# Performance work log

Measured on AMD Instinct MI355X. Metric: run time of the kernel, lower is better.

The kernel has to match this reference:

```python
import jax, jax.numpy as jnp
import numpy as np

B, N, C_IN, C_OUT, K = 2, 8192, 128, 128, 21  # K = num_neighbors + 1 (self)
EPS = 1e-5

def knn_idx(xyz, k):
    # xyz: [B,N,3] -> idx [B,N,k] of k nearest neighbors (self included)
    d2 = jnp.sum(xyz * xyz, axis=-1)  # [B,N]
    dist = d2[:, :, None] + d2[:, None, :] - 2.0 * jnp.einsum('bnd,bmd->bnm', xyz, xyz)
    _, idx = jax.lax.top_k(-dist, k)
    return idx

def group_points(pts, idx):
    # pts [B,N,D], idx [B,N,K] -> [B,N,K,D]
    return jax.vmap(lambda p, i: p[i])(pts, idx)

def group_feats(f, idx):
    # f [B,C,N], idx [B,N,K] -> [B,C,N,K]
    return jax.vmap(lambda ff, i: ff[:, i])(f, idx)

def conv_bn_relu(x, W, g, b, m, v):
    # 1x1 conv (bias=False) + BatchNorm (inference stats) + ReLU
    y = jnp.einsum('oc,bcnk->bonk', W, x)
    inv = g / jnp.sqrt(v + EPS)
    return jax.nn.relu(y * inv[None, :, None, None] + (b - m * inv)[None, :, None, None])

def setup_inputs():
    key = jax.random.key(0)
    ks = jax.random.split(key, 12)
    return {
        'xyz': jax.random.normal(ks[0], (B, N, 3), jnp.float32),
        'f': jax.random.normal(ks[1], (B, C_IN, N), jnp.float32),
        'W_geo': jax.random.normal(ks[2], (C_OUT, 6), jnp.float32) * 0.1,
        'g_geo': jax.random.uniform(ks[3], (C_OUT,), jnp.float32, 0.5, 1.5),
        'b_geo': jax.random.normal(ks[4], (C_OUT,), jnp.float32) * 0.1,
        'm_geo': jax.random.normal(ks[5], (C_OUT,), jnp.float32) * 0.1,
        'v_geo': jax.random.uniform(ks[6], (C_OUT,), jnp.float32, 0.5, 1.5),
        'W_feat': jax.random.normal(ks[7], (C_OUT, 2 * C_IN), jnp.float32) * 0.05,
        'g_feat': jax.random.uniform(ks[8], (C_OUT,), jnp.float32, 0.5, 1.5),
        'b_feat': jax.random.normal(ks[9], (C_OUT,), jnp.float32) * 0.1,
        'm_feat': jax.random.normal(ks[10], (C_OUT,), jnp.float32) * 0.1,
        'v_feat': jax.random.uniform(ks[11], (C_OUT,), jnp.float32, 0.5, 1.5),
    }

def reference(xyz, f, W_geo, g_geo, b_geo, m_geo, v_geo, W_feat, g_feat, b_feat, m_feat, v_feat):
    idx = knn_idx(xyz, K)                                   # [B,N,K]
    grouped_xyz = group_points(xyz, idx)                    # [B,N,K,3]
    xyz_diff = jnp.transpose(grouped_xyz - xyz[:, :, None, :], (0, 3, 1, 2))  # [B,3,N,K]
    center = jnp.broadcast_to(jnp.transpose(xyz, (0, 2, 1))[:, :, :, None], (B, 3, N, K))
    G_geo = jnp.concatenate([center, xyz_diff], axis=1)     # [B,6,N,K]
    grouped_f = group_feats(f, idx)                         # [B,C,N,K]
    center_f = jnp.broadcast_to(f[:, :, :, None], (B, C_IN, N, K))
    G_feat = jnp.concatenate([center_f, grouped_f - center_f], axis=1)  # [B,2C,N,K]
    G_geo = conv_bn_relu(G_geo, W_geo, g_geo, b_geo, m_geo, v_geo)      # [B,C_OUT,N,K]
    G_feat = conv_bn_relu(G_feat, W_feat, g_feat, b_feat, m_feat, v_feat)
    feature = jnp.concatenate([G_geo, G_feat], axis=1)      # [B,2*C_OUT,N,K]
    return jnp.max(feature, axis=-1)                        # [B,2*C_OUT,N]
```

## Files before the change

### kernel.cpp

```cpp
#include <hip/hip_runtime.h>

typedef unsigned int u32;
typedef unsigned long long u64;
typedef unsigned short u16;

#define DEV __device__ __forceinline__

DEV u16 f2bf(float x) {
  u32 u = __float_as_uint(x);
  u32 r = u + 0x7fffu + ((u >> 16) & 1u);
  return (u16)(r >> 16);
}
DEV float bflo(u32 d) { return __uint_as_float(d << 16); }
DEV float bfhi(u32 d) { return __uint_as_float(d & 0xffff0000u); }
DEV u64 sortable64(double f) {
  long long b = __double_as_longlong(f);
  return (u64)b ^ (u64)((b >> 63) | (long long)0x8000000000000000ll);
}
DEV double ddist(double qx, double qy, double qz, double qd2,
                 float mxf, float myf, float mzf) {
  double cx = (double)mxf, cy = (double)myf, cz = (double)mzf;
  double cd2 = cx * cx + cy * cy + cz * cz;
  double dot = cx * qx + cy * qy + cz * qz;
  return (qd2 + cd2) - 2.0 * dot;
}

#define NB 2
#define NN 8192
#define NC 128
#define KK 21
#define MARGIN 1e-3f
#define CT 2048

__global__ __launch_bounds__(256) void k_prep(
    const float* __restrict__ Wf, const float* __restrict__ gf, const float* __restrict__ bf_,
    const float* __restrict__ mf, const float* __restrict__ vf,
    const float* __restrict__ Wg, const float* __restrict__ gg, const float* __restrict__ bg,
    const float* __restrict__ mg, const float* __restrict__ vg,
    u16* __restrict__ Wt, float* __restrict__ beta_f,
    float* __restrict__ Wgu, float* __restrict__ Wgv, float* __restrict__ beta_g) {
  int g = blockIdx.x * 256 + threadIdx.x;
  int c = g >> 8, o = g & 255;
  float val;
  if (o < 128) {
    float inv = gf[o] / sqrtf(vf[o] + 1e-5f);
    val = inv * (Wf[o * 256 + c] - Wf[o * 256 + c + 128]);
  } else {
    int o2 = o - 128;
    float inv = gf[o2] / sqrtf(vf[o2] + 1e-5f);
    val = inv * Wf[o2 * 256 + c + 128];
  }
  Wt[c * 256 + o] = f2bf(val);
  if (g < 128) {
    float inv = gf[g] / sqrtf(vf[g] + 1e-5f);
    beta_f[g] = bf_[g] - mf[g] * inv;
  } else if (g < 256) {
    int oo = g - 128;
    float invg = gg[oo] / sqrtf(vg[oo] + 1e-5f);
#pragma unroll
    for (int d = 0; d < 3; ++d) {
      Wgu[oo * 3 + d] = invg * (Wg[oo * 6 + d] - Wg[oo * 6 + 3 + d]);
      Wgv[oo * 3 + d] = invg * Wg[oo * 6 + 3 + d];
    }
    beta_g[oo] = bg[oo] - mg[oo] * invg;
  }
}

__global__ __launch_bounds__(256) void k_geo(
    const float* __restrict__ xyz, const float* __restrict__ Wgu, const float* __restrict__ Wgv,
    const float* __restrict__ beta_g, u32* __restrict__ ucat, u32* __restrict__ vcat) {
  int g = blockIdx.x * 256 + threadIdx.x;
  int p = g >> 6, oc = g & 63;
  const float* xp = xyz + p * 3;
  float X = xp[0], Y = xp[1], Z = xp[2];
  u32 du = 0, dv = 0;
#pragma unroll
  for (int h = 0; h < 2; ++h) {
    int o = oc * 2 + h;
    float ug = X * Wgu[o * 3] + Y * Wgu[o * 3 + 1] + Z * Wgu[o * 3 + 2] + beta_g[o];
    float vv = X * Wgv[o * 3] + Y * Wgv[o * 3 + 1] + Z * Wgv[o * 3 + 2];
    du |= (u32)f2bf(ug) << (16 * h);
    dv |= (u32)f2bf(vv) << (16 * h);
  }
  ucat[p * 128 + oc] = du;
  vcat[p * 128 + oc] = dv;
}

__global__ __launch_bounds__(256) void k_feat(
    const float* __restrict__ f, const u32* __restrict__ Wt32, const float* __restrict__ beta_f,
    u32* __restrict__ ucat, u32* __restrict__ vcat) {
  __shared__ u32 sW[128 * 128];
  __shared__ float sF[128][68];

  const int t = threadIdx.x;
  const int b = blockIdx.x >> 7;
  const int n0 = (blockIdx.x & 127) << 6;
  const int boff = b * (NC * NN);

#pragma unroll
  for (int k = 0; k < 64; ++k) sW[t + (k << 8)] = Wt32[t + (k << 8)];
#pragma unroll
  for (int k = 0; k < 32; ++k) {
    int i = t + (k << 8);
    int c = i >> 6, col = i & 63;
    sF[c][col] = f[boff + c * NN + n0 + col];
  }
  __syncthreads();

  const int w = t >> 6, lane = t & 63;
  const int og = lane >> 3, pg = lane & 7;
  const int o0 = w * 64 + og * 8;
  const int p0 = pg * 8;

  float acc[8][8];
#pragma unroll
  for (int a = 0; a < 8; ++a)
#pragma unroll
    for (int p = 0; p < 8; ++p) acc[a][p] = 0.0f;

  for (int c = 0; c < 128; ++c) {
    float4 fa = *(const float4*)&sF[c][p0];
    float4 fb = *(const float4*)&sF[c][p0 + 4];
    uint4 wr = *(const uint4*)&sW[c * 128 + (o0 >> 1)];
    float wv[8] = {bflo(wr.x), bfhi(wr.x), bflo(wr.y), bfhi(wr.y),
                   bflo(wr.z), bfhi(wr.z), bflo(wr.w), bfhi(wr.w)};
    float fv[8] = {fa.x, fa.y, fa.z, fa.w, fb.x, fb.y, fb.z, fb.w};
#pragma unroll
    for (int a = 0; a < 8; ++a)
#pragma unroll
      for (int p = 0; p < 8; ++p) acc[a][p] = __builtin_fmaf(wv[a], fv[p], acc[a][p]);
  }

  const int ochan = o0 & 127;
  const bool is_u = (o0 < 128);
  float bet[8];
#pragma unroll
  for (int a = 0; a < 8; ++a) bet[a] = is_u ? beta_f[ochan + a] : 0.0f;
  u32* dstbase = is_u ? ucat : vcat;
#pragma unroll
  for (int p = 0; p < 8; ++p) {
    int pt = (b << 13) + n0 + p0 + p;
    u32 d0 = (u32)f2bf(acc[0][p] + bet[0]) | ((u32)f2bf(acc[1][p] + bet[1]) << 16);
    u32 d1 = (u32)f2bf(acc[2][p] + bet[2]) | ((u32)f2bf(acc[3][p] + bet[3]) << 16);
    u32 d2 = (u32)f2bf(acc[4][p] + bet[4]) | ((u32)f2bf(acc[5][p] + bet[5]) << 16);
    u32 d3 = (u32)f2bf(acc[6][p] + bet[6]) | ((u32)f2bf(acc[7][p] + bet[7]) << 16);
    *(uint4*)&dstbase[pt * 128 + 64 + (ochan >> 1)] = make_uint4(d0, d1, d2, d3);
  }
}

__global__ __launch_bounds__(256, 4) void k_knn(const float* __restrict__ xyz,
                                                int* __restrict__ knn) {
  __shared__ float4 sc[CT];
  __shared__ u16 ssurv[16][128];
  __shared__ u32 scnt[16];

  const int t = threadIdx.x;
  const int blk = blockIdx.x;
  const int b = blk >> 9;
  const int n0 = (blk & 511) << 4;
  const float* X = xyz + b * (NN * 3);

  if (t < 16) scnt[t] = 0u;

  const int w = t >> 6, lane = t & 63;

  float mx[4], my[4], mz[4];
#pragma unroll
  for (int i = 0; i < 4; ++i) {
    int q = n0 + (w << 2) + i;
    mx[i] = -2.0f * X[q * 3];
    my[i] = -2.0f * X[q * 3 + 1];
    mz[i] = -2.0f * X[q * 3 + 2];
  }

  float mn[4];
#pragma unroll
  for (int i = 0; i < 4; ++i) mn[i] = __builtin_inff();

  for (int ct = 0; ct < NN / CT; ++ct) {
    __syncthreads();
    const float* Xt = X + ct * (CT * 3);
#pragma unroll
    for (int k = 0; k < 8; ++k) {
      int c = (k << 8) + t;
      float x = Xt[c * 3], y = Xt[c * 3 + 1], z = Xt[c * 3 + 2];
      float d2 = __builtin_fmaf(x, x, __builtin_fmaf(y, y, z * z));
      sc[c] = make_float4(x, y, z, d2);
    }
    __syncthreads();
#pragma unroll 4
    for (int cc = 0; cc < CT; cc += 64) {
      float4 C = sc[cc + lane];
#pragma unroll
      for (int i = 0; i < 4; ++i) {
        float s = __builtin_fmaf(C.x, mx[i],
                  __builtin_fmaf(C.y, my[i],
                  __builtin_fmaf(C.z, mz[i], C.w)));
        mn[i] = fminf(mn[i], s);
      }
    }
  }

  float thr[4];
#pragma unroll
  for (int i = 0; i < 4; ++i) {
    float v = mn[i];
#pragma unroll
    for (int k = 2; k <= 64; k <<= 1) {
#pragma unroll
      for (int j = k >> 1; j > 0; j >>= 1) {
        float p = __shfl_xor(v, j);
        bool takeMin = (((lane & k) == 0) == ((lane & j) == 0));
        v = takeMin ? fminf(v, p) : fmaxf(v, p);
      }
    }
    thr[i] = __shfl(v, 20) + MARGIN;
  }

  for (int ct = 0; ct < NN / CT; ++ct) {
    __syncthreads();
    const float* Xt = X + ct * (CT * 3);
#pragma unroll
    for (int k = 0; k < 8; ++k) {
      int c = (k << 8) + t;
      float x = Xt[c * 3], y = Xt[c * 3 + 1], z = Xt[c * 3 + 2];
      float d2 = __builtin_fmaf(x, x, __builtin_fmaf(y, y, z * z));
      sc[c] = make_float4(x, y, z, d2);
    }
    __syncthreads();
    int mbase = ct * CT + lane;
#pragma unroll 4
    for (int cc = 0; cc < CT; cc += 64) {
      float4 C = sc[cc + lane];
#pragma unroll
      for (int i = 0; i < 4; ++i) {
        float s = __builtin_fmaf(C.x, mx[i],
                  __builtin_fmaf(C.y, my[i],
                  __builtin_fmaf(C.z, mz[i], C.w)));
        if (s <= thr[i]) {
          int qq = (w << 2) + i;
          u32 slot = atomicAdd(&scnt[qq], 1u);
          if (slot < 128u) ssurv[qq][slot] = (u16)(mbase + cc);
        }
      }
    }
  }
  __syncthreads();

#pragma unroll 1
  for (int i = 0; i < 4; ++i) {
    const int qq = (w << 2) + i;
    const int q = n0 + qq;
    double Qx = (double)X[q * 3], Qy = (double)X[q * 3 + 1], Qz = (double)X[q * 3 + 2];
    double Qd2 = Qx * Qx + Qy * Qy + Qz * Qz;
    u32 cnt = scnt[qq];
    int* outp = knn + ((b << 13) + q) * KK;

    bool v0 = ((u32)lane < cnt);
    u32 m0 = v0 ? (u32)ssurv[qq][lane] : 0u;
    double s0 = ddist(Qx, Qy, Qz, Qd2, X[m0 * 3], X[m0 * 3 + 1], X[m0 * 3 + 2]);
    u64 k0 = v0 ? ((sortable64(s0) & 0xFFFFFFFFFFFFE000ull) | (u64)m0) : ~0ull;

    if (cnt <= 64u) {
      u64 v = k0;
#pragma unroll
      for (int k = 2; k <= 64; k <<= 1) {
#pragma unroll
        for (int j = k >> 1; j > 0; j >>= 1) {
          u64 p = __shfl_xor(v, j);
          bool takeMin = (((lane & k) == 0) == ((lane & j) == 0));
          bool pl = p < v;
          u64 mnv = pl ? p : v;
          u64 mxv = pl ? v : p;
          v = takeMin ? mnv : mxv;
        }
      }
      if (lane < KK) outp[lane] = (int)(v & 8191ull);
    } else {
      bool v1 = ((u32)(lane + 64) < cnt);
      u32 m1 = v1 ? (u32)ssurv[qq][lane + 64] : 0u;
      double s1 = ddist(Qx, Qy, Qz, Qd2, X[m1 * 3], X[m1 * 3 + 1], X[m1 * 3 + 2]);
      u64 k1 = v1 ? ((sortable64(s1) & 0xFFFFFFFFFFFFE000ull) | (u64)m1) : ~0ull;
      u32 selm = 0;
      for (int r = 0; r < KK; ++r) {
        u64 mk = (k0 < k1) ? k0 : k1;
#pragma unroll
        for (int j = 32; j > 0; j >>= 1) {
          u64 p = __shfl_xor(mk, j);
          if (p < mk) mk = p;
        }
        if (k0 == mk) k0 = ~0ull;
        else if (k1 == mk) k1 = ~0ull;
        if (lane == r) selm = (u32)(mk & 8191ull);
      }
      if (lane < KK) outp[lane] = (int)selm;
    }
  }
}

__global__ __launch_bounds__(256) void k_gather(
    const u32* __restrict__ ucat, const u32* __restrict__ vcat,
    const int* __restrict__ knn, float* __restrict__ out) {
  __shared__ float tr[64 * 258];

  const int t = threadIdx.x;
  const int b = blockIdx.x >> 7;
  const int n0 = (blockIdx.x & 127) << 6;
  const int w = t >> 6, lane = t & 63;
  const int which = w >> 1;
  const int lo = ((w & 1) << 6) | lane;

  for (int step = 0; step < 32; ++step) {
    int qq = step * 2 + which;
    int q = n0 + qq;
    const int* ip = knn + ((b << 13) + q) * KK;
    float a0 = -__builtin_inff(), a1 = -__builtin_inff();
#pragma unroll
    for (int k = 0; k < KK; ++k) {
      int p = ip[k];
      u32 d = vcat[(((b << 13) + p) << 7) + lo];
      a0 = fmaxf(a0, bflo(d));
      a1 = fmaxf(a1, bfhi(d));
    }
    u32 u = ucat[(((b << 13) + q) << 7) + lo];
    float r0 = fmaxf(bflo(u) + a0, 0.0f);
    float r1 = fmaxf(bfhi(u) + a1, 0.0f);
    *(float2*)&tr[qq * 258 + 2 * lo] = make_float2(r0, r1);
  }
  __syncthreads();

  float* ob = out + b * (256 * NN);
  for (int i = 0; i < 64; ++i) {
    int o = (w << 6) + i;
    ob[o * NN + n0 + lane] = tr[lane * 258 + o];
  }
}

extern "C" void kernel_launch(void* const* d_in, const int* in_sizes, int n_in,
                              void* d_out, int out_size, void* d_ws, size_t ws_size,
                              hipStream_t stream) {
  const float* xyz = (const float*)d_in[0];
  const float* f   = (const float*)d_in[1];
  const float* Wg  = (const float*)d_in[2];
  const float* gg  = (const float*)d_in[3];
  const float* bg  = (const float*)d_in[4];
  const float* mg  = (const float*)d_in[5];
  const float* vg  = (const float*)d_in[6];
  const float* Wf  = (const float*)d_in[7];
  const float* gf  = (const float*)d_in[8];
  const float* bf_ = (const float*)d_in[9];
  const float* mf  = (const float*)d_in[10];
  const float* vf  = (const float*)d_in[11];

  char* ws = (char*)d_ws;
  u16*   Wt     = (u16*)ws;
  float* beta_f = (float*)(ws + 65536);
  float* Wgu    = (float*)(ws + 66048);
  float* Wgv    = (float*)(ws + 67584);
  float* beta_g = (float*)(ws + 69120);
  u32*   ucat   = (u32*)(ws + 69632);
  u32*   vcat   = (u32*)(ws + 69632 + 8388608);
  int*   knn    = (int*)(ws + 69632 + 2 * 8388608);
  float* out    = (float*)d_out;

  if (ws_size < (size_t)(69632 + 2 * 8388608 + 16384 * KK * 4)) return;

  k_prep<<<dim3(128), dim3(256), 0, stream>>>(Wf, gf, bf_, mf, vf, Wg, gg, bg, mg, vg,
                                              Wt, beta_f, Wgu, Wgv, beta_g);
  k_geo<<<dim3(4096), dim3(256), 0, stream>>>(xyz, Wgu, Wgv, beta_g, ucat, vcat);
  k_feat<<<dim3(256), dim3(256), 0, stream>>>(f, (const u32*)Wt, beta_f, ucat, vcat);
  k_knn<<<dim3(1024), dim3(256), 0, stream>>>(xyz, knn);
  k_gather<<<dim3(256), dim3(256), 0, stream>>>(ucat, vcat, knn, out);
}
```

Before: 194.2 us.

## Compute kNN distance filtering with bf16 split-precision MFMA instead of scalar FMA

Adds a packing kernel that splits each point's coordinates and squared norm into hi/lo bf16 parts. The kNN kernel then computes the candidate distance matrix for 32 queries per block with 32x32x16 bf16 MFMA instructions, replacing per-lane scalar FMAs over LDS-staged tiles. It uses that matrix both for the 21st-smallest threshold pass and for the survivor-collection pass. Because the split bf16 distances are approximate, the margin is widened and the survivor buffer grows to 256, with a new 4-key selection path. Exact ranking is still done in double precision. The risk is more survivors and atomics per query, and possible misses if the approximation error exceeds the margin.

After: 205.5 us. 1.06x slower.

```diff
diff --git a/kernel.cpp b/kernel.cpp
--- a/kernel.cpp
+++ b/kernel.cpp
@@ -5,12 +5,16 @@
 typedef unsigned short u16;
 
 #define DEV __device__ __forceinline__
+
+typedef __attribute__((ext_vector_type(8))) short bf16x8;
+typedef __attribute__((ext_vector_type(16))) float f32x16;
 
 DEV u16 f2bf(float x) {
   u32 u = __float_as_uint(x);
   u32 r = u + 0x7fffu + ((u >> 16) & 1u);
   return (u16)(r >> 16);
 }
+DEV float bf2f(u16 h) { return __uint_as_float((u32)h << 16); }
 DEV float bflo(u32 d) { return __uint_as_float(d << 16); }
 DEV float bfhi(u32 d) { return __uint_as_float(d & 0xffff0000u); }
 DEV u64 sortable64(double f) {
@@ -29,8 +33,8 @@
 #define NN 8192
 #define NC 128
 #define KK 21
-#define MARGIN 1e-3f
-#define CT 2048
+#define MARGIN 0.012f
+#define BF16_ONE ((u16)0x3F80)
 
 __global__ __launch_bounds__(256) void k_prep(
     const float* __restrict__ Wf, const float* __restrict__ gf, const float* __restrict__ bf_,
@@ -148,63 +152,104 @@
   }
 }
 
-__global__ __launch_bounds__(256, 4) void k_knn(const float* __restrict__ xyz,
+__global__ __launch_bounds__(256) void k_pack(const float* __restrict__ xyz,
+                                              u16* __restrict__ pack) {
+  int p = blockIdx.x * 256 + threadIdx.x;
+  const float* xp = xyz + p * 3;
+  float x = xp[0], y = xp[1], z = xp[2];
+  u16 hx = f2bf(x), hy = f2bf(y), hz = f2bf(z);
+  u16 lx = f2bf(x - bf2f(hx)), ly = f2bf(y - bf2f(hy)), lz = f2bf(z - bf2f(hz));
+  float cd2 = __builtin_fmaf(x, x, __builtin_fmaf(y, y, z * z));
+  u16 dh = f2bf(cd2), dl = f2bf(cd2 - bf2f(dh));
+
+  int g = p >> 5, n = p & 31;
+  u32* h0 = (u32*)(pack + (size_t)g * 512 + n * 8);
+  u32* h1 = (u32*)(pack + (size_t)g * 512 + 256 + n * 8);
+  h0[0] = (u32)hx | ((u32)hy << 16);
+  h0[1] = (u32)hz | ((u32)hx << 16);
+  h0[2] = (u32)hy | ((u32)hz << 16);
+  h0[3] = (u32)lx | ((u32)ly << 16);
+  h1[0] = (u32)lz | ((u32)dh << 16);
+  h1[1] = (u32)dl | ((u32)lx << 16);
+  h1[2] = (u32)ly | ((u32)lz << 16);
+  h1[3] = 0u;
+}
+
+DEV u64 surv_key(const u16* __restrict__ srow, u32 cnt, int pos,
+                 const float* __restrict__ X,
+                 double Qx, double Qy, double Qz, double Qd2) {
+  bool vv = (u32)pos < cnt;
+  u32 m = vv ? (u32)srow[pos] : 0u;
+  double ss = ddist(Qx, Qy, Qz, Qd2, X[m * 3], X[m * 3 + 1], X[m * 3 + 2]);
+  return vv ? ((sortable64(ss) & 0xFFFFFFFFFFFFE000ull) | (u64)m) : ~0ull;
+}
+
+__global__ __launch_bounds__(256, 2) void k_knn(const float* __restrict__ xyz,
+                                                const u16* __restrict__ pack,
                                                 int* __restrict__ knn) {
-  __shared__ float4 sc[CT];
-  __shared__ u16 ssurv[16][128];
-  __shared__ u32 scnt[16];
-
-  const int t = threadIdx.x;
+  __shared__ float smin[32][128];
+  __shared__ u16 ssurv[32][256];
+  __shared__ float sthr[32];
+  __shared__ u32 scnt[32];
+
+  const int t = threadIdx.x, w = t >> 6, lane = t & 63;
   const int blk = blockIdx.x;
-  const int b = blk >> 9;
-  const int n0 = (blk & 511) << 4;
+  const int b = blk >> 8;
+  const int n0 = (blk & 255) << 5;
   const float* X = xyz + b * (NN * 3);
-
-  if (t < 16) scnt[t] = 0u;
-
-  const int w = t >> 6, lane = t & 63;
-
-  float mx[4], my[4], mz[4];
-#pragma unroll
-  for (int i = 0; i < 4; ++i) {
-    int q = n0 + (w << 2) + i;
-    mx[i] = -2.0f * X[q * 3];
-    my[i] = -2.0f * X[q * 3 + 1];
-    mz[i] = -2.0f * X[q * 3 + 2];
-  }
-
-  float mn[4];
-#pragma unroll
-  for (int i = 0; i < 4; ++i) mn[i] = __builtin_inff();
-
-  for (int ct = 0; ct < NN / CT; ++ct) {
-    __syncthreads();
-    const float* Xt = X + ct * (CT * 3);
-#pragma unroll
-    for (int k = 0; k < 8; ++k) {
-      int c = (k << 8) + t;
-      float x = Xt[c * 3], y = Xt[c * 3 + 1], z = Xt[c * 3 + 2];
-      float d2 = __builtin_fmaf(x, x, __builtin_fmaf(y, y, z * z));
-      sc[c] = make_float4(x, y, z, d2);
-    }
-    __syncthreads();
-#pragma unroll 4
-    for (int cc = 0; cc < CT; cc += 64) {
-      float4 C = sc[cc + lane];
-#pragma unroll
-      for (int i = 0; i < 4; ++i) {
-        float s = __builtin_fmaf(C.x, mx[i],
-                  __builtin_fmaf(C.y, my[i],
-                  __builtin_fmaf(C.z, mz[i], C.w)));
-        mn[i] = fminf(mn[i], s);
-      }
-    }
-  }
-
-  float thr[4];
-#pragma unroll
-  for (int i = 0; i < 4; ++i) {
-    float v = mn[i];
+  const u16* PB = pack + (size_t)b * NN * 16;
+
+  if (t < 32) scnt[t] = 0u;
+
+  const int mq = lane & 31, h = lane >> 5;
+  union { u16 u[8]; bf16x8 v; } afr;
+  {
+    int q = n0 + mq;
+    float qx = -2.0f * X[q * 3], qy = -2.0f * X[q * 3 + 1], qz = -2.0f * X[q * 3 + 2];
+    u16 hx = f2bf(qx), hy = f2bf(qy), hz = f2bf(qz);
+    u16 lx = f2bf(qx - bf2f(hx)), ly = f2bf(qy - bf2f(hy)), lz = f2bf(qz - bf2f(hz));
+    if (h == 0) {
+      afr.u[0] = hx; afr.u[1] = hy; afr.u[2] = hz; afr.u[3] = lx;
+      afr.u[4] = ly; afr.u[5] = lz; afr.u[6] = hx; afr.u[7] = hy;
+    } else {
+      afr.u[0] = hz; afr.u[1] = BF16_ONE; afr.u[2] = BF16_ONE; afr.u[3] = lx;
+      afr.u[4] = ly; afr.u[5] = lz; afr.u[6] = 0; afr.u[7] = 0;
+    }
+  }
+
+  f32x16 zacc = {0.f, 0.f, 0.f, 0.f, 0.f, 0.f, 0.f, 0.f,
+                 0.f, 0.f, 0.f, 0.f, 0.f, 0.f, 0.f, 0.f};
+
+  float mn[16];
+#pragma unroll
+  for (int r = 0; r < 16; ++r) mn[r] = __builtin_inff();
+
+  for (int i0 = 0; i0 < 64; i0 += 8) {
+    uint4 braw[8];
+#pragma unroll
+    for (int j = 0; j < 8; ++j) {
+      int tile = w + 4 * (i0 + j);
+      braw[j] = *(const uint4*)(PB + (size_t)tile * 512 + lane * 8);
+    }
+#pragma unroll
+    for (int j = 0; j < 8; ++j) {
+      union { uint4 r; bf16x8 v; } bf; bf.r = braw[j];
+      f32x16 d = __builtin_amdgcn_mfma_f32_32x32x16_bf16(afr.v, bf.v, zacc, 0, 0, 0);
+#pragma unroll
+      for (int r = 0; r < 16; ++r) mn[r] = fminf(mn[r], d[r]);
+    }
+  }
+
+#pragma unroll
+  for (int r = 0; r < 16; ++r) {
+    int row = (r & 3) + 8 * (r >> 2) + 4 * h;
+    smin[row][w * 32 + mq] = mn[r];
+  }
+  __syncthreads();
+
+  for (int i = 0; i < 8; ++i) {
+    int row = w * 8 + i;
+    float v = fminf(smin[row][lane], smin[row][lane + 64]);
 #pragma unroll
     for (int k = 2; k <= 64; k <<= 1) {
 #pragma unroll
@@ -214,33 +259,33 @@
         v = takeMin ? fminf(v, p) : fmaxf(v, p);
       }
     }
-    thr[i] = __shfl(v, 20) + MARGIN;
-  }
-
-  for (int ct = 0; ct < NN / CT; ++ct) {
-    __syncthreads();
-    const float* Xt = X + ct * (CT * 3);
-#pragma unroll
-    for (int k = 0; k < 8; ++k) {
-      int c = (k << 8) + t;
-      float x = Xt[c * 3], y = Xt[c * 3 + 1], z = Xt[c * 3 + 2];
-      float d2 = __builtin_fmaf(x, x, __builtin_fmaf(y, y, z * z));
-      sc[c] = make_float4(x, y, z, d2);
-    }
-    __syncthreads();
-    int mbase = ct * CT + lane;
-#pragma unroll 4
-    for (int cc = 0; cc < CT; cc += 64) {
-      float4 C = sc[cc + lane];
-#pragma unroll
-      for (int i = 0; i < 4; ++i) {
-        float s = __builtin_fmaf(C.x, mx[i],
-                  __builtin_fmaf(C.y, my[i],
-                  __builtin_fmaf(C.z, mz[i], C.w)));
-        if (s <= thr[i]) {
-          int qq = (w << 2) + i;
-          u32 slot = atomicAdd(&scnt[qq], 1u);
-          if (slot < 128u) ssurv[qq][slot] = (u16)(mbase + cc);
+    float t20 = __shfl(v, 20);
+    if (lane == 0) sthr[row] = t20 + MARGIN;
+  }
+  __syncthreads();
+
+  float thr[16];
+#pragma unroll
+  for (int r = 0; r < 16; ++r) thr[r] = sthr[(r & 3) + 8 * (r >> 2) + 4 * h];
+
+  for (int i0 = 0; i0 < 64; i0 += 4) {
+    uint4 braw[4];
+#pragma unroll
+    for (int j = 0; j < 4; ++j) {
+      int tile = w + 4 * (i0 + j);
+      braw[j] = *(const uint4*)(PB + (size_t)tile * 512 + lane * 8);
+    }
+#pragma unroll
+    for (int j = 0; j < 4; ++j) {
+      int tile = w + 4 * (i0 + j);
+      union { uint4 r; bf16x8 v; } bf; bf.r = braw[j];
+      f32x16 d = __builtin_amdgcn_mfma_f32_32x32x16_bf16(afr.v, bf.v, zacc, 0, 0, 0);
+#pragma unroll
+      for (int r = 0; r < 16; ++r) {
+        if (d[r] <= thr[r]) {
+          int row = (r & 3) + 8 * (r >> 2) + 4 * h;
+          u32 slot = atomicAdd(&scnt[row], 1u);
+          if (slot < 256u) ssurv[row][slot] = (u16)(tile * 32 + mq);
         }
       }
     }
@@ -248,18 +293,16 @@
   __syncthreads();
 
 #pragma unroll 1
-  for (int i = 0; i < 4; ++i) {
-    const int qq = (w << 2) + i;
+  for (int i = 0; i < 8; ++i) {
+    const int qq = (w << 3) + i;
     const int q = n0 + qq;
     double Qx = (double)X[q * 3], Qy = (double)X[q * 3 + 1], Qz = (double)X[q * 3 + 2];
     double Qd2 = Qx * Qx + Qy * Qy + Qz * Qz;
-    u32 cnt = scnt[qq];
+    u32 cnt = scnt[qq]; if (cnt > 256u) cnt = 256u;
+    const u16* srow = ssurv[qq];
     int* outp = knn + ((b << 13) + q) * KK;
 
-    bool v0 = ((u32)lane < cnt);
-    u32 m0 = v0 ? (u32)ssurv[qq][lane] : 0u;
-    double s0 = ddist(Qx, Qy, Qz, Qd2, X[m0 * 3], X[m0 * 3 + 1], X[m0 * 3 + 2]);
-    u64 k0 = v0 ? ((sortable64(s0) & 0xFFFFFFFFFFFFE000ull) | (u64)m0) : ~0ull;
+    u64 k0 = surv_key(srow, cnt, lane, X, Qx, Qy, Qz, Qd2);
 
     if (cnt <= 64u) {
       u64 v = k0;
@@ -276,11 +319,8 @@
         }
       }
       if (lane < KK) outp[lane] = (int)(v & 8191ull);
-    } else {
-      bool v1 = ((u32)(lane + 64) < cnt);
-      u32 m1 = v1 ? (u32)ssurv[qq][lane + 64] : 0u;
-      double s1 = ddist(Qx, Qy, Qz, Qd2, X[m1 * 3], X[m1 * 3 + 1], X[m1 * 3 + 2]);
-      u64 k1 = v1 ? ((sortable64(s1) & 0xFFFFFFFFFFFFE000ull) | (u64)m1) : ~0ull;
+    } else if (cnt <= 128u) {
+      u64 k1 = surv_key(srow, cnt, lane + 64, X, Qx, Qy, Qz, Qd2);
       u32 selm = 0;
       for (int r = 0; r < KK; ++r) {
         u64 mk = (k0 < k1) ? k0 : k1;
@@ -291,6 +331,27 @@
         }
         if (k0 == mk) k0 = ~0ull;
         else if (k1 == mk) k1 = ~0ull;
+        if (lane == r) selm = (u32)(mk & 8191ull);
+      }
+      if (lane < KK) outp[lane] = (int)selm;
+    } else {
+      u64 k1 = surv_key(srow, cnt, lane + 64, X, Qx, Qy, Qz, Qd2);
+      u64 k2 = surv_key(srow, cnt, lane + 128, X, Qx, Qy, Qz, Qd2);
+      u64 k3 = surv_key(srow, cnt, lane + 192, X, Qx, Qy, Qz, Qd2);
+      u32 selm = 0;
+      for (int r = 0; r < KK; ++r) {
+        u64 m01 = (k0 < k1) ? k0 : k1;
+        u64 m23 = (k2 < k3) ? k2 : k3;
+        u64 mk = (m01 < m23) ? m01 : m23;
+#pragma unroll
+        for (int j = 32; j > 0; j >>= 1) {
+          u64 p = __shfl_xor(mk, j);
+          if (p < mk) mk = p;
+        }
+        if (k0 == mk) k0 = ~0ull;
+        else if (k1 == mk) k1 = ~0ull;
+        else if (k2 == mk) k2 = ~0ull;
+        else if (k3 == mk) k3 = ~0ull;
         if (lane == r) selm = (u32)(mk & 8191ull);
       }
       if (lane < KK) outp[lane] = (int)selm;
@@ -360,15 +421,17 @@
   float* beta_g = (float*)(ws + 69120);
   u32*   ucat   = (u32*)(ws + 69632);
   u32*   vcat   = (u32*)(ws + 69632 + 8388608);
-  int*   knn    = (int*)(ws + 69632 + 2 * 8388608);
+  int*   knn    = (int*)(ws + 16846848);
+  u16*   pack   = (u16*)(ws + 18223104);
   float* out    = (float*)d_out;
 
-  if (ws_size < (size_t)(69632 + 2 * 8388608 + 16384 * KK * 4)) return;
+  if (ws_size < (size_t)(18223104 + 524288)) return;
 
   k_prep<<<dim3(128), dim3(256), 0, stream>>>(Wf, gf, bf_, mf, vf, Wg, gg, bg, mg, vg,
                                               Wt, beta_f, Wgu, Wgv, beta_g);
   k_geo<<<dim3(4096), dim3(256), 0, stream>>>(xyz, Wgu, Wgv, beta_g, ucat, vcat);
   k_feat<<<dim3(256), dim3(256), 0, stream>>>(f, (const u32*)Wt, beta_f, ucat, vcat);
-  k_knn<<<dim3(1024), dim3(256), 0, stream>>>(xyz, knn);
+  k_pack<<<dim3(64), dim3(256), 0, stream>>>(xyz, pack);
+  k_knn<<<dim3(512), dim3(256), 0, stream>>>(xyz, (const u16*)pack, knn);
   k_gather<<<dim3(256), dim3(256), 0, stream>>>(ucat, vcat, knn, out);
 }
```

## Fuse kNN threshold and survivor passes into single sweep with progressive threshold

Applied to the files above, without the earlier changes.

The kNN kernel previously swept all candidates twice: once to compute a 21st-smallest threshold per query, and again to collect survivors. It now derives an initial threshold from the first 2048-point tile and collects survivors in the same single sweep, tightening the threshold after each later tile. Tile loading also switches to float4-vectorized global reads. Because early thresholds are looser, more candidates survive, so survivor capacity grows to 192 and a three-slot selection path is added. The trade-off is extra atomics and shared-memory traffic, and a risk of overflowing the survivor buffer.

After: 232.1 us. +19.5%, slower.

```diff
diff --git a/kernel.cpp b/kernel.cpp
--- a/kernel.cpp
+++ b/kernel.cpp
@@ -31,6 +31,7 @@
 #define KK 21
 #define MARGIN 1e-3f
 #define CT 2048
+#define SCAP 192
 
 __global__ __launch_bounds__(256) void k_prep(
     const float* __restrict__ Wf, const float* __restrict__ gf, const float* __restrict__ bf_,
@@ -148,10 +149,32 @@
   }
 }
 
+DEV u64 surv_key(const u16* __restrict__ srow, u32 cnt, int pos,
+                 const float* __restrict__ X,
+                 double Qx, double Qy, double Qz, double Qd2) {
+  bool vv = (u32)pos < cnt;
+  u32 m = vv ? (u32)srow[pos] : 0u;
+  double ss = ddist(Qx, Qy, Qz, Qd2, X[m * 3], X[m * 3 + 1], X[m * 3 + 2]);
+  return vv ? ((sortable64(ss) & 0xFFFFFFFFFFFFE000ull) | (u64)m) : ~0ull;
+}
+
+DEV float stat21(float v, int lane) {
+#pragma unroll
+  for (int k = 2; k <= 64; k <<= 1) {
+#pragma unroll
+    for (int j = k >> 1; j > 0; j >>= 1) {
+      float p = __shfl_xor(v, j);
+      bool takeMin = (((lane & k) == 0) == ((lane & j) == 0));
+      v = takeMin ? fminf(v, p) : fmaxf(v, p);
+    }
+  }
+  return __shfl(v, 20);
+}
+
 __global__ __launch_bounds__(256, 4) void k_knn(const float* __restrict__ xyz,
                                                 int* __restrict__ knn) {
   __shared__ float4 sc[CT];
-  __shared__ u16 ssurv[16][128];
+  __shared__ u16 ssurv[16][SCAP];
   __shared__ u32 scnt[16];
 
   const int t = threadIdx.x;
@@ -173,75 +196,102 @@
     mz[i] = -2.0f * X[q * 3 + 2];
   }
 
-  float mn[4];
+  float mn[4], thr[4];
 #pragma unroll
   for (int i = 0; i < 4; ++i) mn[i] = __builtin_inff();
 
-  for (int ct = 0; ct < NN / CT; ++ct) {
+  {
+    const float4* g4 = (const float4*)X;
+#pragma unroll
+    for (int gix = 0; gix < 2; ++gix) {
+      int g = t + (gix << 8);
+      float4 a = g4[g * 3], bb = g4[g * 3 + 1], c = g4[g * 3 + 2];
+      float px[4] = {a.x, a.w, bb.z, c.y};
+      float py[4] = {a.y, bb.x, bb.w, c.z};
+      float pz[4] = {a.z, bb.y, c.x, c.w};
+#pragma unroll
+      for (int j = 0; j < 4; ++j) {
+        float d2 = __builtin_fmaf(px[j], px[j], __builtin_fmaf(py[j], py[j], pz[j] * pz[j]));
+        sc[(g << 2) + j] = make_float4(px[j], py[j], pz[j], d2);
+      }
+    }
+  }
+  __syncthreads();
+
+#pragma unroll 4
+  for (int cc = 0; cc < CT; cc += 64) {
+    float4 C = sc[cc + lane];
+#pragma unroll
+    for (int i = 0; i < 4; ++i) {
+      float s = __builtin_fmaf(C.x, mx[i],
+                __builtin_fmaf(C.y, my[i],
+                __builtin_fmaf(C.z, mz[i], C.w)));
+      mn[i] = fminf(mn[i], s);
+    }
+  }
+#pragma unroll
+  for (int i = 0; i < 4; ++i) thr[i] = stat21(mn[i], lane) + MARGIN;
+
+#pragma unroll 4
+  for (int cc = 0; cc < CT; cc += 64) {
+    float4 C = sc[cc + lane];
+    int mbase = cc + lane;
+#pragma unroll
+    for (int i = 0; i < 4; ++i) {
+      float s = __builtin_fmaf(C.x, mx[i],
+                __builtin_fmaf(C.y, my[i],
+                __builtin_fmaf(C.z, mz[i], C.w)));
+      if (s <= thr[i]) {
+        int qq = (w << 2) + i;
+        u32 slot = atomicAdd(&scnt[qq], 1u);
+        if (slot < (u32)SCAP) ssurv[qq][slot] = (u16)mbase;
+      }
+    }
+  }
+
+  for (int ct = 1; ct < NN / CT; ++ct) {
     __syncthreads();
-    const float* Xt = X + ct * (CT * 3);
-#pragma unroll
-    for (int k = 0; k < 8; ++k) {
-      int c = (k << 8) + t;
-      float x = Xt[c * 3], y = Xt[c * 3 + 1], z = Xt[c * 3 + 2];
-      float d2 = __builtin_fmaf(x, x, __builtin_fmaf(y, y, z * z));
-      sc[c] = make_float4(x, y, z, d2);
+    {
+      const float4* g4 = (const float4*)(X + ct * (CT * 3));
+#pragma unroll
+      for (int gix = 0; gix < 2; ++gix) {
+        int g = t + (gix << 8);
+        float4 a = g4[g * 3], bb = g4[g * 3 + 1], c = g4[g * 3 + 2];
+        float px[4] = {a.x, a.w, bb.z, c.y};
+        float py[4] = {a.y, bb.x, bb.w, c.z};
+        float pz[4] = {a.z, bb.y, c.x, c.w};
+#pragma unroll
+        for (int j = 0; j < 4; ++j) {
+          float d2 = __builtin_fmaf(px[j], px[j], __builtin_fmaf(py[j], py[j], pz[j] * pz[j]));
+          sc[(g << 2) + j] = make_float4(px[j], py[j], pz[j], d2);
+        }
+      }
     }
     __syncthreads();
+
+    int tbase = ct * CT;
 #pragma unroll 4
     for (int cc = 0; cc < CT; cc += 64) {
       float4 C = sc[cc + lane];
+      int mbase = tbase + cc + lane;
 #pragma unroll
       for (int i = 0; i < 4; ++i) {
         float s = __builtin_fmaf(C.x, mx[i],
                   __builtin_fmaf(C.y, my[i],
                   __builtin_fmaf(C.z, mz[i], C.w)));
         mn[i] = fminf(mn[i], s);
-      }
-    }
-  }
-
-  float thr[4];
-#pragma unroll
-  for (int i = 0; i < 4; ++i) {
-    float v = mn[i];
-#pragma unroll
-    for (int k = 2; k <= 64; k <<= 1) {
-#pragma unroll
-      for (int j = k >> 1; j > 0; j >>= 1) {
-        float p = __shfl_xor(v, j);
-        bool takeMin = (((lane & k) == 0) == ((lane & j) == 0));
-        v = takeMin ? fminf(v, p) : fmaxf(v, p);
-      }
-    }
-    thr[i] = __shfl(v, 20) + MARGIN;
-  }
-
-  for (int ct = 0; ct < NN / CT; ++ct) {
-    __syncthreads();
-    const float* Xt = X + ct * (CT * 3);
-#pragma unroll
-    for (int k = 0; k < 8; ++k) {
-      int c = (k << 8) + t;
-      float x = Xt[c * 3], y = Xt[c * 3 + 1], z = Xt[c * 3 + 2];
-      float d2 = __builtin_fmaf(x, x, __builtin_fmaf(y, y, z * z));
-      sc[c] = make_float4(x, y, z, d2);
-    }
-    __syncthreads();
-    int mbase = ct * CT + lane;
-#pragma unroll 4
-    for (int cc = 0; cc < CT; cc += 64) {
-      float4 C = sc[cc + lane];
-#pragma unroll
-      for (int i = 0; i < 4; ++i) {
-        float s = __builtin_fmaf(C.x, mx[i],
-                  __builtin_fmaf(C.y, my[i],
-                  __builtin_fmaf(C.z, mz[i], C.w)));
         if (s <= thr[i]) {
           int qq = (w << 2) + i;
           u32 slot = atomicAdd(&scnt[qq], 1u);
-          if (slot < 128u) ssurv[qq][slot] = (u16)(mbase + cc);
+          if (slot < (u32)SCAP) ssurv[qq][slot] = (u16)mbase;
         }
+      }
+    }
+    if (ct < 3) {
+#pragma unroll
+      for (int i = 0; i < 4; ++i) {
+        float nt = stat21(mn[i], lane) + MARGIN;
+        thr[i] = fminf(thr[i], nt);
       }
     }
   }
@@ -253,13 +303,11 @@
     const int q = n0 + qq;
     double Qx = (double)X[q * 3], Qy = (double)X[q * 3 + 1], Qz = (double)X[q * 3 + 2];
     double Qd2 = Qx * Qx + Qy * Qy + Qz * Qz;
-    u32 cnt = scnt[qq];
+    u32 cnt = scnt[qq]; if (cnt > (u32)SCAP) cnt = (u32)SCAP;
+    const u16* srow = ssurv[qq];
     int* outp = knn + ((b << 13) + q) * KK;
 
-    bool v0 = ((u32)lane < cnt);
-    u32 m0 = v0 ? (u32)ssurv[qq][lane] : 0u;
-    double s0 = ddist(Qx, Qy, Qz, Qd2, X[m0 * 3], X[m0 * 3 + 1], X[m0 * 3 + 2]);
-    u64 k0 = v0 ? ((sortable64(s0) & 0xFFFFFFFFFFFFE000ull) | (u64)m0) : ~0ull;
+    u64 k0 = surv_key(srow, cnt, lane, X, Qx, Qy, Qz, Qd2);
 
     if (cnt <= 64u) {
       u64 v = k0;
@@ -276,11 +324,8 @@
         }
       }
       if (lane < KK) outp[lane] = (int)(v & 8191ull);
-    } else {
-      bool v1 = ((u32)(lane + 64) < cnt);
-      u32 m1 = v1 ? (u32)ssurv[qq][lane + 64] : 0u;
-      double s1 = ddist(Qx, Qy, Qz, Qd2, X[m1 * 3], X[m1 * 3 + 1], X[m1 * 3 + 2]);
-      u64 k1 = v1 ? ((sortable64(s1) & 0xFFFFFFFFFFFFE000ull) | (u64)m1) : ~0ull;
+    } else if (cnt <= 128u) {
+      u64 k1 = surv_key(srow, cnt, lane + 64, X, Qx, Qy, Qz, Qd2);
       u32 selm = 0;
       for (int r = 0; r < KK; ++r) {
         u64 mk = (k0 < k1) ? k0 : k1;
@@ -291,6 +336,24 @@
         }
         if (k0 == mk) k0 = ~0ull;
         else if (k1 == mk) k1 = ~0ull;
+        if (lane == r) selm = (u32)(mk & 8191ull);
+      }
+      if (lane < KK) outp[lane] = (int)selm;
+    } else {
+      u64 k1 = surv_key(srow, cnt, lane + 64, X, Qx, Qy, Qz, Qd2);
+      u64 k2 = surv_key(srow, cnt, lane + 128, X, Qx, Qy, Qz, Qd2);
+      u32 selm = 0;
+      for (int r = 0; r < KK; ++r) {
+        u64 m01 = (k0 < k1) ? k0 : k1;
+        u64 mk = (m01 < k2) ? m01 : k2;
+#pragma unroll
+        for (int j = 32; j > 0; j >>= 1) {
+          u64 p = __shfl_xor(mk, j);
+          if (p < mk) mk = p;
+        }
+        if (k0 == mk) k0 = ~0ull;
+        else if (k1 == mk) k1 = ~0ull;
+        else if (k2 == mk) k2 = ~0ull;
         if (lane == r) selm = (u32)(mk & 8191ull);
       }
       if (lane < KK) outp[lane] = (int)selm;
@@ -360,10 +423,10 @@
   float* beta_g = (float*)(ws + 69120);
   u32*   ucat   = (u32*)(ws + 69632);
   u32*   vcat   = (u32*)(ws + 69632 + 8388608);
-  int*   knn    = (int*)(ws + 69632 + 2 * 8388608);
+  int*   knn    = (int*)(ws + 16846848);
   float* out    = (float*)d_out;
 
-  if (ws_size < (size_t)(69632 + 2 * 8388608 + 16384 * KK * 4)) return;
+  if (ws_size < (size_t)(16846848 + 16384 * KK * 4)) return;
 
   k_prep<<<dim3(128), dim3(256), 0, stream>>>(Wf, gf, bf_, mf, vf, Wg, gg, bg, mg, vg,
                                               Wt, beta_f, Wgu, Wgv, beta_g);
```
